# Performance work log

Measured on AMD Instinct MI355X. Metric: run time of the kernel, lower is better.

Reference implementation:

```python
import jax, jax.numpy as jnp
import numpy as np

N_NODES = 50000
N_EDGES = 200000
D_IN = 512
D_OUT = 512

def setup_inputs() -> dict:
    key = jax.random.key(0)
    k1, k2, k3, k4, k5, k6 = jax.random.split(key, 6)
    h = jax.random.normal(k1, (N_NODES, D_IN), dtype=jnp.float32)
    W = jax.random.normal(k2, (D_IN, D_OUT), dtype=jnp.float32) * (1.0 / np.sqrt(D_IN))
    b = jax.random.normal(k3, (D_OUT,), dtype=jnp.float32) * 0.01
    edge_weight = jax.random.uniform(k4, (N_EDGES,), dtype=jnp.float32)
    src = jax.random.randint(k5, (N_EDGES,), 0, N_NODES, dtype=jnp.int32)
    dst = jax.random.randint(k6, (N_EDGES,), 0, N_NODES, dtype=jnp.int32)
    return {"h": h, "W": W, "b": b, "edge_weight": edge_weight, "src": src, "dst": dst}

def reference(h, W, b, edge_weight, src, dst):
    # Linear projection of source-node features (nn.Linear)
    h_proj = h @ W + b                                   # [N, D_OUT]
    # u_mul_e: gather projected src features, scale by scalar edge weight
    msg = h_proj[src] * edge_weight[:, None]             # [E, D_OUT]
    # mean aggregation over incoming edges per destination node (DGL fn.mean)
    sums = jax.ops.segment_sum(msg, dst, num_segments=N_NODES)          # [N, D_OUT]
    cnt = jax.ops.segment_sum(jnp.ones_like(edge_weight), dst, num_segments=N_NODES)  # [N]
    agg = sums / jnp.maximum(cnt, 1.0)[:, None]          # zero-in-degree nodes -> 0
    # ReLU then dropout (eval mode -> identity)
    return jax.nn.relu(agg)
```

## Files before the change

kernel.cpp:

```cpp
#include <hip/hip_runtime.h>

#define NNODES 50000
#define NEDGES 200000
#define DDIM 512

typedef __attribute__((ext_vector_type(8))) short bf16x8;
typedef __attribute__((ext_vector_type(4))) float f32x4;

static __device__ __forceinline__ unsigned short f2bf(float f) {
  unsigned u = __float_as_uint(f);
  unsigned r = (u + 0x7fffu + ((u >> 16) & 1u)) >> 16;
  return (unsigned short)r;
}

static __device__ __forceinline__ void gload_lds16(const void* g, void* l) {
  __builtin_amdgcn_global_load_lds(
      (const __attribute__((address_space(1))) unsigned int*)g,
      (__attribute__((address_space(3))) unsigned int*)l, 16, 0, 0);
}

__global__ __launch_bounds__(256) void cvt_h_kernel(
    const float* __restrict__ in, unsigned short* __restrict__ out, int n8) {
  for (int i = blockIdx.x * 256 + threadIdx.x; i < n8; i += gridDim.x * 256) {
    const float4 v0 = ((const float4*)in)[(size_t)i * 2];
    const float4 v1 = ((const float4*)in)[(size_t)i * 2 + 1];
    uint4 p;
    p.x = (unsigned)f2bf(v0.x) | ((unsigned)f2bf(v0.y) << 16);
    p.y = (unsigned)f2bf(v0.z) | ((unsigned)f2bf(v0.w) << 16);
    p.z = (unsigned)f2bf(v1.x) | ((unsigned)f2bf(v1.y) << 16);
    p.w = (unsigned)f2bf(v1.z) | ((unsigned)f2bf(v1.w) << 16);
    ((uint4*)out)[i] = p;
  }
}

__global__ __launch_bounds__(256) void cvt_wt_kernel(
    const float* __restrict__ W, unsigned short* __restrict__ Wt) {
  __shared__ float t[32][33];
  const int n0 = blockIdx.x * 32, k0 = blockIdx.y * 32;
  const int tx = threadIdx.x & 31, ty = threadIdx.x >> 5;
  for (int r = ty; r < 32; r += 8)
    t[r][tx] = W[(size_t)(k0 + r) * DDIM + n0 + tx];
  __syncthreads();
  for (int r = ty; r < 32; r += 8)
    Wt[(size_t)(n0 + r) * DDIM + k0 + tx] = f2bf(t[tx][r]);
}

__global__ __launch_bounds__(256) void gemm_mfma_kernel(
    const unsigned short* __restrict__ Ab, const unsigned short* __restrict__ Bt,
    const float* __restrict__ bias, unsigned short* __restrict__ C, int M) {
  __shared__ unsigned short As[2][128 * 32];
  __shared__ unsigned short Bs[2][128 * 32];
  const int tid = threadIdx.x;
  const int wid = tid >> 6, lane = tid & 63;

  const int nwg = gridDim.x;
  const int q = nwg >> 3, rr = nwg & 7;
  const int x = blockIdx.x & 7, idx = blockIdx.x >> 3;
  const int wg = x * q + min(x, rr) + idx;

  const int mt = wg >> 2, nt = wg & 3;
  const int bm = mt * 128, bn = nt * 128;
  const int wr = wid >> 1, wc = wid & 1;

  f32x4 acc[4][4] = {};

  const int r0 = tid >> 2;
  const int cge = (tid & 3) ^ ((r0 >> 1) & 3);

  const int arow0 = min(bm + r0, M - 1);
  const int arow1 = min(bm + r0 + 64, M - 1);

  const unsigned short* a0 = Ab + (size_t)arow0 * DDIM + cge * 8;
  const unsigned short* a1 = Ab + (size_t)arow1 * DDIM + cge * 8;
  const unsigned short* b0 = Bt + (size_t)(bn + r0) * DDIM + cge * 8;
  const unsigned short* b1 = Bt + (size_t)(bn + r0 + 64) * DDIM + cge * 8;

  const int l16 = lane & 15, lk = lane >> 4;
  const int lke = lk ^ ((l16 >> 1) & 3);

  const int sOff0 = (wid * 64) * 8;
  const int sOff1 = (256 + wid * 64) * 8;

#define STAGE(buf, k0)                        \
  do {                                        \
    gload_lds16(a0 + (k0), &As[buf][sOff0]);  \
    gload_lds16(a1 + (k0), &As[buf][sOff1]);  \
    gload_lds16(b0 + (k0), &Bs[buf][sOff0]);  \
    gload_lds16(b1 + (k0), &Bs[buf][sOff1]);  \
  } while (0)

#define COMPUTE(buf)                                                          \
  do {                                                                        \
    bf16x8 af[4], bfr[4];                                                     \
    _Pragma("unroll") for (int i = 0; i < 4; ++i) {                           \
      af[i]  = *(const bf16x8*)&As[buf][(wr * 64 + i * 16 + l16) * 32 + lke * 8]; \
      bfr[i] = *(const bf16x8*)&Bs[buf][(wc * 64 + i * 16 + l16) * 32 + lke * 8]; \
    }                                                                         \
    _Pragma("unroll") for (int i = 0; i < 4; ++i)                             \
        _Pragma("unroll") for (int j = 0; j < 4; ++j)                         \
            acc[i][j] = __builtin_amdgcn_mfma_f32_16x16x32_bf16(              \
                af[i], bfr[j], acc[i][j], 0, 0, 0);                           \
  } while (0)

  STAGE(0, 0);
  __syncthreads();
#pragma unroll 2
  for (int t = 0; t < 15; ++t) {
    const int cur = t & 1;
    STAGE(cur ^ 1, (t + 1) * 32);
    COMPUTE(cur);
    __syncthreads();
  }
  COMPUTE(1);
  __syncthreads();

  unsigned short* cl = (wid < 2) ? &As[0][0] + wid * 4096
                                 : &Bs[0][0] + (wid - 2) * 4096;
#pragma unroll
  for (int j = 0; j < 4; ++j) {
    const float bv = bias[bn + wc * 64 + j * 16 + l16];
#pragma unroll
    for (int i = 0; i < 4; ++i)
#pragma unroll
      for (int qq = 0; qq < 4; ++qq)
        cl[(i * 16 + lk * 4 + qq) * 64 + j * 16 + l16] =
            f2bf(acc[i][j][qq] + bv);
  }
  __syncthreads();
#pragma unroll
  for (int pass = 0; pass < 8; ++pass) {
    const int rt = pass * 8 + (lane >> 3);
    const int c0 = (lane & 7) * 8;
    const int grow = bm + wr * 64 + rt;
    if (grow < M) {
      const uint4 v = *(const uint4*)&cl[rt * 64 + c0];
      *(uint4*)&C[(size_t)grow * DDIM + bn + wc * 64 + c0] = v;
    }
  }
#undef STAGE
#undef COMPUTE
}

__global__ __launch_bounds__(256) void hist_kernel(const int* __restrict__ dst,
                                                   int* __restrict__ deg, int E) {
  const int e = blockIdx.x * 256 + threadIdx.x;
  if (e < E) atomicAdd(&deg[dst[e]], 1);
}

__global__ __launch_bounds__(256) void chunk_sum_kernel(
    const int* __restrict__ deg, int* __restrict__ part, int n) {
  const int base = blockIdx.x * 1024;
  int v = 0;
  for (int i = threadIdx.x; i < 1024; i += 256) {
    const int idx = base + i;
    v += (idx < n) ? deg[idx] : 0;
  }
#pragma unroll
  for (int s = 32; s; s >>= 1) v += __shfl_down(v, s, 64);
  __shared__ int ws[4];
  if ((threadIdx.x & 63) == 0) ws[threadIdx.x >> 6] = v;
  __syncthreads();
  if (threadIdx.x == 0) part[blockIdx.x] = ws[0] + ws[1] + ws[2] + ws[3];
}

__global__ void scan_part_kernel(int* __restrict__ part, int nb) {
  const int lane = threadIdx.x & 63;
  int v = (lane < nb) ? part[lane] : 0;
  int incl = v;
#pragma unroll
  for (int s = 1; s < 64; s <<= 1) {
    int t = __shfl_up(incl, s, 64);
    if (lane >= s) incl += t;
  }
  if (lane < nb) part[lane] = incl - v;
}

__global__ __launch_bounds__(1024) void chunk_scan_kernel(
    const int* __restrict__ deg, const int* __restrict__ part,
    int* __restrict__ off, int* __restrict__ cur, int n) {
  __shared__ int wsum[16];
  const int tid = threadIdx.x, lane = tid & 63, wid = tid >> 6;
  const int i = blockIdx.x * 1024 + tid;
  const int v = (i < n) ? deg[i] : 0;
  int incl = v;
#pragma unroll
  for (int s = 1; s < 64; s <<= 1) {
    int t = __shfl_up(incl, s, 64);
    if (lane >= s) incl += t;
  }
  if (lane == 63) wsum[wid] = incl;
  __syncthreads();
  if (wid == 0 && lane < 16) {
    int wv = wsum[lane];
#pragma unroll
    for (int s = 1; s < 16; s <<= 1) {
      int t = __shfl_up(wv, s, 16);
      if (lane >= s) wv += t;
    }
    wsum[lane] = wv;
  }
  __syncthreads();
  const int add = part[blockIdx.x] + ((wid > 0) ? wsum[wid - 1] : 0);
  if (i < n) {
    off[i + 1] = add + incl;
    cur[i] = add + incl - v;
  }
  if (i == 0) off[0] = 0;
}

__global__ __launch_bounds__(256) void fill_kernel(
    const int* __restrict__ src, const int* __restrict__ dst,
    const float* __restrict__ ew, int* __restrict__ cur,
    uint2* __restrict__ epair, int E) {
  const int e = blockIdx.x * 256 + threadIdx.x;
  if (e >= E) return;
  const int p = atomicAdd(&cur[dst[e]], 1);
  epair[p] = make_uint2((unsigned)src[e], __float_as_uint(ew[e]));
}

__global__ __launch_bounds__(256) void gather_kernel(
    const unsigned short* __restrict__ hp, const int* __restrict__ off,
    const uint2* __restrict__ epair, float* __restrict__ out, int n) {
  const int node = blockIdx.x * 4 + (threadIdx.x >> 6);
  if (node >= n) return;
  const int lane = threadIdx.x & 63;
  const int beg = off[node], end = off[node + 1];

  float acc[8] = {0.f, 0.f, 0.f, 0.f, 0.f, 0.f, 0.f, 0.f};
  int p = beg;
  for (; p + 2 <= end; p += 2) {
    const uint2 e0 = epair[p];
    const uint2 e1 = epair[p + 1];
    const float w0 = __uint_as_float(e0.y);
    const float w1 = __uint_as_float(e1.y);
    const uint4 u0 = *(const uint4*)(hp + (size_t)e0.x * DDIM + lane * 8);
    const uint4 u1 = *(const uint4*)(hp + (size_t)e1.x * DDIM + lane * 8);
    const unsigned a0[4] = {u0.x, u0.y, u0.z, u0.w};
    const unsigned a1[4] = {u1.x, u1.y, u1.z, u1.w};
#pragma unroll
    for (int qv = 0; qv < 4; ++qv) {
      acc[2 * qv + 0] += w0 * __uint_as_float(a0[qv] << 16) +
                         w1 * __uint_as_float(a1[qv] << 16);
      acc[2 * qv + 1] += w0 * __uint_as_float(a0[qv] & 0xffff0000u) +
                         w1 * __uint_as_float(a1[qv] & 0xffff0000u);
    }
  }
  if (p < end) {
    const uint2 e0 = epair[p];
    const float w0 = __uint_as_float(e0.y);
    const uint4 u0 = *(const uint4*)(hp + (size_t)e0.x * DDIM + lane * 8);
    const unsigned a0[4] = {u0.x, u0.y, u0.z, u0.w};
#pragma unroll
    for (int qv = 0; qv < 4; ++qv) {
      acc[2 * qv + 0] += w0 * __uint_as_float(a0[qv] << 16);
      acc[2 * qv + 1] += w0 * __uint_as_float(a0[qv] & 0xffff0000u);
    }
  }

  const float inv = 1.0f / fmaxf((float)(end - beg), 1.0f);
  float4 o0, o1;
  o0.x = fmaxf(acc[0] * inv, 0.f);
  o0.y = fmaxf(acc[1] * inv, 0.f);
  o0.z = fmaxf(acc[2] * inv, 0.f);
  o0.w = fmaxf(acc[3] * inv, 0.f);
  o1.x = fmaxf(acc[4] * inv, 0.f);
  o1.y = fmaxf(acc[5] * inv, 0.f);
  o1.z = fmaxf(acc[6] * inv, 0.f);
  o1.w = fmaxf(acc[7] * inv, 0.f);
  float* orow = out + (size_t)node * DDIM + lane * 8;
  *(float4*)(orow + 0) = o0;
  *(float4*)(orow + 4) = o1;
}

extern "C" void kernel_launch(void* const* d_in, const int* in_sizes, int n_in,
                              void* d_out, int out_size, void* d_ws, size_t ws_size,
                              hipStream_t stream) {
  const float* h  = (const float*)d_in[0];
  const float* W  = (const float*)d_in[1];
  const float* b  = (const float*)d_in[2];
  const float* ew = (const float*)d_in[3];
  const int* src  = (const int*)d_in[4];
  const int* dst  = (const int*)d_in[5];
  float* out = (float*)d_out;

  unsigned short* hb = (unsigned short*)d_out;
  unsigned short* Wt = (unsigned short*)((char*)d_out + (size_t)NNODES * DDIM * 2);

  char* ws = (char*)d_ws;
  size_t o = 0;
  auto alloc = [&](size_t bytes) {
    char* p = ws + o;
    o += (bytes + 255) & ~(size_t)255;
    return p;
  };
  unsigned short* hp = (unsigned short*)alloc((size_t)NNODES * DDIM * 2);
  int* deg    = (int*)alloc((size_t)NNODES * 4);
  int* off    = (int*)alloc((size_t)(NNODES + 1) * 4);
  int* cur    = (int*)alloc((size_t)NNODES * 4);
  uint2* epair = (uint2*)alloc((size_t)NEDGES * 8);
  int* part   = (int*)alloc(64 * 4);

  const int nchunks = (NNODES + 1023) / 1024;

  cvt_h_kernel<<<2048, 256, 0, stream>>>(h, hb, NNODES * DDIM / 8);
  dim3 wgrid(16, 16);
  cvt_wt_kernel<<<wgrid, 256, 0, stream>>>(W, Wt);

  const int mtiles = (NNODES + 127) / 128;
  gemm_mfma_kernel<<<mtiles * 4, 256, 0, stream>>>(hb, Wt, b, hp, NNODES);

  hipMemsetAsync(deg, 0, (size_t)NNODES * 4, stream);
  hist_kernel<<<(NEDGES + 255) / 256, 256, 0, stream>>>(dst, deg, NEDGES);
  chunk_sum_kernel<<<nchunks, 256, 0, stream>>>(deg, part, NNODES);
  scan_part_kernel<<<1, 64, 0, stream>>>(part, nchunks);
  chunk_scan_kernel<<<nchunks, 1024, 0, stream>>>(deg, part, off, cur, NNODES);
  fill_kernel<<<(NEDGES + 255) / 256, 256, 0, stream>>>(src, dst, ew, cur,
                                                        epair, NEDGES);

  gather_kernel<<<(NNODES + 3) / 4, 256, 0, stream>>>(hp, off, epair, out,
                                                      NNODES);
}
```

Baseline: 150.1 us.

## Fuse fp32-to-bf16 conversion of h into GEMM A-tile staging

```diff
diff --git a/kernel.cpp b/kernel.cpp
--- a/kernel.cpp
+++ b/kernel.cpp
@@ -19,22 +19,12 @@
       (__attribute__((address_space(3))) unsigned int*)l, 16, 0, 0);
 }
 
-__global__ __launch_bounds__(256) void cvt_h_kernel(
-    const float* __restrict__ in, unsigned short* __restrict__ out, int n8) {
-  for (int i = blockIdx.x * 256 + threadIdx.x; i < n8; i += gridDim.x * 256) {
-    const float4 v0 = ((const float4*)in)[(size_t)i * 2];
-    const float4 v1 = ((const float4*)in)[(size_t)i * 2 + 1];
-    uint4 p;
-    p.x = (unsigned)f2bf(v0.x) | ((unsigned)f2bf(v0.y) << 16);
-    p.y = (unsigned)f2bf(v0.z) | ((unsigned)f2bf(v0.w) << 16);
-    p.z = (unsigned)f2bf(v1.x) | ((unsigned)f2bf(v1.y) << 16);
-    p.w = (unsigned)f2bf(v1.z) | ((unsigned)f2bf(v1.w) << 16);
-    ((uint4*)out)[i] = p;
-  }
-}
-
 __global__ __launch_bounds__(256) void cvt_wt_kernel(
-    const float* __restrict__ W, unsigned short* __restrict__ Wt) {
+    const float* __restrict__ W, unsigned short* __restrict__ Wt,
+    int* __restrict__ deg) {
+  const int gid = (blockIdx.x + blockIdx.y * gridDim.x) * 256 + threadIdx.x;
+  if (gid < NNODES) deg[gid] = 0;
+
   __shared__ float t[32][33];
   const int n0 = blockIdx.x * 32, k0 = blockIdx.y * 32;
   const int tx = threadIdx.x & 31, ty = threadIdx.x >> 5;
@@ -46,7 +36,7 @@
 }
 
 __global__ __launch_bounds__(256) void gemm_mfma_kernel(
-    const unsigned short* __restrict__ Ab, const unsigned short* __restrict__ Bt,
+    const float* __restrict__ A, const unsigned short* __restrict__ Bt,
     const float* __restrict__ bias, unsigned short* __restrict__ C, int M) {
   __shared__ unsigned short As[2][128 * 32];
   __shared__ unsigned short Bs[2][128 * 32];
@@ -70,8 +60,8 @@
   const int arow0 = min(bm + r0, M - 1);
   const int arow1 = min(bm + r0 + 64, M - 1);
 
-  const unsigned short* a0 = Ab + (size_t)arow0 * DDIM + cge * 8;
-  const unsigned short* a1 = Ab + (size_t)arow1 * DDIM + cge * 8;
+  const float* ha0 = A + (size_t)arow0 * DDIM + cge * 8;
+  const float* ha1 = A + (size_t)arow1 * DDIM + cge * 8;
   const unsigned short* b0 = Bt + (size_t)(bn + r0) * DDIM + cge * 8;
   const unsigned short* b1 = Bt + (size_t)(bn + r0 + 64) * DDIM + cge * 8;
 
@@ -81,10 +71,33 @@
   const int sOff0 = (wid * 64) * 8;
   const int sOff1 = (256 + wid * 64) * 8;
 
-#define STAGE(buf, k0)                        \
+  float4 ra00, ra01, ra10, ra11;
+
+#define STAGE_A_LOAD(kf)                           \
+  do {                                             \
+    ra00 = *(const float4*)(ha0 + (kf));           \
+    ra01 = *(const float4*)(ha0 + (kf) + 4);       \
+    ra10 = *(const float4*)(ha1 + (kf));           \
+    ra11 = *(const float4*)(ha1 + (kf) + 4);       \
+  } while (0)
+
+#define STAGE_A_WRITE(buf)                                              \
+  do {                                                                  \
+    uint4 p0, p1;                                                       \
+    p0.x = (unsigned)f2bf(ra00.x) | ((unsigned)f2bf(ra00.y) << 16);     \
+    p0.y = (unsigned)f2bf(ra00.z) | ((unsigned)f2bf(ra00.w) << 16);     \
+    p0.z = (unsigned)f2bf(ra01.x) | ((unsigned)f2bf(ra01.y) << 16);     \
+    p0.w = (unsigned)f2bf(ra01.z) | ((unsigned)f2bf(ra01.w) << 16);     \
+    p1.x = (unsigned)f2bf(ra10.x) | ((unsigned)f2bf(ra10.y) << 16);     \
+    p1.y = (unsigned)f2bf(ra10.z) | ((unsigned)f2bf(ra10.w) << 16);     \
+    p1.z = (unsigned)f2bf(ra11.x) | ((unsigned)f2bf(ra11.y) << 16);     \
+    p1.w = (unsigned)f2bf(ra11.z) | ((unsigned)f2bf(ra11.w) << 16);     \
+    *(uint4*)&As[buf][(size_t)tid * 8] = p0;                            \
+    *(uint4*)&As[buf][(size_t)(256 + tid) * 8] = p1;                    \
+  } while (0)
+
+#define STAGE_B(buf, k0)                      \
   do {                                        \
-    gload_lds16(a0 + (k0), &As[buf][sOff0]);  \
-    gload_lds16(a1 + (k0), &As[buf][sOff1]);  \
     gload_lds16(b0 + (k0), &Bs[buf][sOff0]);  \
     gload_lds16(b1 + (k0), &Bs[buf][sOff1]);  \
   } while (0)
@@ -102,13 +115,18 @@
                 af[i], bfr[j], acc[i][j], 0, 0, 0);                           \
   } while (0)
 
-  STAGE(0, 0);
-  __syncthreads();
+  STAGE_A_LOAD(0);
+  STAGE_B(0, 0);
+  STAGE_A_WRITE(0);
+  __syncthreads();
+
 #pragma unroll 2
   for (int t = 0; t < 15; ++t) {
     const int cur = t & 1;
-    STAGE(cur ^ 1, (t + 1) * 32);
+    STAGE_A_LOAD((t + 1) * 32);
+    STAGE_B(cur ^ 1, (t + 1) * 32);
     COMPUTE(cur);
+    STAGE_A_WRITE(cur ^ 1);
     __syncthreads();
   }
   COMPUTE(1);
@@ -137,7 +155,9 @@
       *(uint4*)&C[(size_t)grow * DDIM + bn + wc * 64 + c0] = v;
     }
   }
-#undef STAGE
+#undef STAGE_A_LOAD
+#undef STAGE_A_WRITE
+#undef STAGE_B
 #undef COMPUTE
 }
 
@@ -258,7 +278,7 @@
   }
 
   const float inv = 1.0f / fmaxf((float)(end - beg), 1.0f);
-  float4 o0, o1;
+  f32x4 o0, o1;
   o0.x = fmaxf(acc[0] * inv, 0.f);
   o0.y = fmaxf(acc[1] * inv, 0.f);
   o0.z = fmaxf(acc[2] * inv, 0.f);
@@ -268,8 +288,8 @@
   o1.z = fmaxf(acc[6] * inv, 0.f);
   o1.w = fmaxf(acc[7] * inv, 0.f);
   float* orow = out + (size_t)node * DDIM + lane * 8;
-  *(float4*)(orow + 0) = o0;
-  *(float4*)(orow + 4) = o1;
+  __builtin_nontemporal_store(o0, (f32x4*)(orow + 0));
+  __builtin_nontemporal_store(o1, (f32x4*)(orow + 4));
 }
 
 extern "C" void kernel_launch(void* const* d_in, const int* in_sizes, int n_in,
@@ -283,9 +303,6 @@
   const int* dst  = (const int*)d_in[5];
   float* out = (float*)d_out;
 
-  unsigned short* hb = (unsigned short*)d_out;
-  unsigned short* Wt = (unsigned short*)((char*)d_out + (size_t)NNODES * DDIM * 2);
-
   char* ws = (char*)d_ws;
   size_t o = 0;
   auto alloc = [&](size_t bytes) {
@@ -294,6 +311,7 @@
     return p;
   };
   unsigned short* hp = (unsigned short*)alloc((size_t)NNODES * DDIM * 2);
+  unsigned short* Wt = (unsigned short*)alloc((size_t)DDIM * DDIM * 2);
   int* deg    = (int*)alloc((size_t)NNODES * 4);
   int* off    = (int*)alloc((size_t)(NNODES + 1) * 4);
   int* cur    = (int*)alloc((size_t)NNODES * 4);
@@ -302,14 +320,12 @@
 
   const int nchunks = (NNODES + 1023) / 1024;
 
-  cvt_h_kernel<<<2048, 256, 0, stream>>>(h, hb, NNODES * DDIM / 8);
   dim3 wgrid(16, 16);
-  cvt_wt_kernel<<<wgrid, 256, 0, stream>>>(W, Wt);
+  cvt_wt_kernel<<<wgrid, 256, 0, stream>>>(W, Wt, deg);
 
   const int mtiles = (NNODES + 127) / 128;
-  gemm_mfma_kernel<<<mtiles * 4, 256, 0, stream>>>(hb, Wt, b, hp, NNODES);
-
-  hipMemsetAsync(deg, 0, (size_t)NNODES * 4, stream);
+  gemm_mfma_kernel<<<mtiles * 4, 256, 0, stream>>>(h, Wt, b, hp, NNODES);
+
   hist_kernel<<<(NEDGES + 255) / 256, 256, 0, stream>>>(dst, deg, NEDGES);
   chunk_sum_kernel<<<nchunks, 256, 0, stream>>>(deg, part, NNODES);
   scan_part_kernel<<<1, 64, 0, stream>>>(part, nchunks);
```

After: 154.8 us. 3.2% more time.
